# Performance work log

Measured on AMD Instinct MI355X. Metric: run time of the kernel, lower is better.

The kernel has to match this reference:

```python
import jax, jax.numpy as jnp
import numpy as np
import math

EMBED_DIM = 1024
NUM_HEADS = 16
HEAD_DIM = EMBED_DIM // NUM_HEADS


def setup_inputs() -> dict:
    key = jax.random.key(0)
    ks = jax.random.split(key, 5)
    x = jax.random.normal(ks[0], (4, 2048, EMBED_DIM), dtype=jnp.float32)
    # Linear params (torch nn.Linear: y = x @ W.T + b); init scale ~ 1/sqrt(fan_in)
    s = 1.0 / math.sqrt(EMBED_DIM)
    qkv_w = jax.random.uniform(ks[1], (3 * EMBED_DIM, EMBED_DIM), jnp.float32, -s, s)
    qkv_b = jax.random.uniform(ks[2], (3 * EMBED_DIM,), jnp.float32, -s, s)
    proj_w = jax.random.uniform(ks[3], (EMBED_DIM, EMBED_DIM), jnp.float32, -s, s)
    proj_b = jax.random.uniform(ks[4], (EMBED_DIM,), jnp.float32, -s, s)
    return {"x": x, "qkv_w": qkv_w, "qkv_b": qkv_b, "proj_w": proj_w, "proj_b": proj_b}


def reference(x, qkv_w, qkv_b, proj_w, proj_b):
    bsz, num_tokens, dim = x.shape
    qkv = x @ qkv_w.T + qkv_b  # [B, S, 3*D]
    qkv = qkv.reshape(bsz, num_tokens, 3, NUM_HEADS, HEAD_DIM)
    qkv = jnp.transpose(qkv, (2, 0, 3, 1, 4))  # [3, B, H, S, hd]
    q, k, v = qkv[0], qkv[1], qkv[2]
    scale = 1.0 / math.sqrt(HEAD_DIM)
    attn_scores = jnp.einsum('bhqd,bhkd->bhqk', q, k) * scale  # [B, H, S, S]
    attn = jax.nn.softmax(attn_scores, axis=-1)
    out = jnp.einsum('bhqk,bhkd->bhqd', attn, v)  # [B, H, S, hd]
    out = jnp.transpose(out, (0, 2, 1, 3)).reshape(bsz, num_tokens, dim)
    out = out @ proj_w.T + proj_b
    return out
```

## Files before the change

kernel.cpp:

```cpp
#include <hip/hip_runtime.h>
#include <stdint.h>

#define DEVICE static __device__ __forceinline__

typedef __bf16 bf16x8 __attribute__((ext_vector_type(8)));
typedef float f32x4 __attribute__((ext_vector_type(4)));

#define AS1 __attribute__((address_space(1)))
#define AS3 __attribute__((address_space(3)))

DEVICE void g2l16(const void* gptr, void* lptr) {
  __builtin_amdgcn_global_load_lds((AS1 uint32_t*)(uintptr_t)gptr,
                                   (AS3 uint32_t*)(uint32_t)(uintptr_t)lptr,
                                   16, 0, 0);
}

DEVICE float b2f(ushort h) {
  union { uint32_t u; float f; } v;
  v.u = ((uint32_t)h) << 16;
  return v.f;
}
DEVICE ushort f2b(float f) {
  union { float f; uint32_t u; } v;
  v.f = f;
  uint32_t u = v.u;
  return (ushort)((u + 0x7FFFu + ((u >> 16) & 1u)) >> 16);
}

#if defined(__has_builtin) && __has_builtin(__builtin_amdgcn_exp2f)
DEVICE float fast_exp2(float x) { return __builtin_amdgcn_exp2f(x); }
#else
extern "C" __device__ float __ocml_native_exp2_f32(float);
DEVICE float fast_exp2(float x) { return __ocml_native_exp2_f32(x); }
#endif

#define QSCALE 0.1803368801111244f

DEVICE int kperm(int x) {
  return (x & 0x23) | ((x & 0x18) >> 1) | ((x & 0x4) << 2);
}

__global__ void detect_dtype(const ushort* __restrict__ xu, int* __restrict__ flag) {
  __shared__ int bad;
  if (threadIdx.x == 0) bad = 0;
  __syncthreads();
  int mybad = 0;
#pragma unroll
  for (int j = 0; j < 8; ++j) {
    const int i = threadIdx.x * 8 + j;
    const ushort u = xu[2 * i];
    const int e = (u >> 7) & 0xFF;
    if (!(e == 0 || (e >= 96 && e <= 160))) mybad++;
  }
  atomicAdd(&bad, mybad);
  __syncthreads();
  if (threadIdx.x == 0) *flag = (bad > 512) ? 1 : 0;
}

__global__ void convert_all(const void* __restrict__ s0, const void* __restrict__ s1,
                            const void* __restrict__ s2, const void* __restrict__ s3,
                            const void* __restrict__ s4,
                            ushort* __restrict__ d0, ushort* __restrict__ d1,
                            ushort* __restrict__ d2, ushort* __restrict__ d3,
                            ushort* __restrict__ d4,
                            const int* __restrict__ flag) {
  const bool isf32 = (*flag != 0);
  for (int g = blockIdx.x * blockDim.x + threadIdx.x; g < 1573376;
       g += gridDim.x * blockDim.x) {
    const void* src; ushort* dst; int i;
    if (g < 1048576)      { src = s0; dst = d0; i = g; }
    else if (g < 1441792) { src = s1; dst = d1; i = g - 1048576; }
    else if (g < 1442176) { src = s2; dst = d2; i = g - 1441792; }
    else if (g < 1573248) { src = s3; dst = d3; i = g - 1442176; }
    else                  { src = s4; dst = d4; i = g - 1573248; }
    ushort pk[8];
    if (isf32) {
      const float4 a = ((const float4*)src)[2 * i];
      const float4 b = ((const float4*)src)[2 * i + 1];
      pk[0] = f2b(a.x); pk[1] = f2b(a.y); pk[2] = f2b(a.z); pk[3] = f2b(a.w);
      pk[4] = f2b(b.x); pk[5] = f2b(b.y); pk[6] = f2b(b.z); pk[7] = f2b(b.w);
      *(uint4*)&dst[8 * i] = *(const uint4*)pk;
    } else {
      *(uint4*)&dst[8 * i] = ((const uint4*)src)[i];
    }
  }
}

template <int MODE, int GN>
__global__ __launch_bounds__(512, 4)
void gemm256(const ushort* __restrict__ A, const ushort* __restrict__ W,
             const ushort* __restrict__ bias, ushort* __restrict__ O0,
             ushort* __restrict__ O1, ushort* __restrict__ O2,
             int M, int N, int K, const int* __restrict__ flag)
{
  __shared__ __align__(16) char smem[49152];

  const int tid = threadIdx.x;
  const int lane = tid & 63;
  const int wave = tid >> 6;
  const int quad = lane >> 4;
  const int lo = lane & 15;
  const int kch = (quad ^ ((lo >> 1) & 3)) << 3;

  const int lin = blockIdx.y * gridDim.x + blockIdx.x;
  const int per = GN * gridDim.y;
  const int grp = lin / per;
  const int w   = lin % per;
  const int bxn = grp * GN + (w % GN);
  const int bym = w / GN;
  const int m0 = bym * 128;
  const int n0 = bxn * 256;

  const int wm = (wave >> 2) * 64;
  const int wn = (wave & 3) * 64;

  const int rA = tid >> 2;
  const int gA = (((tid & 3) ^ ((tid >> 3) & 3)) << 3);
  const size_t offA  = (size_t)(m0 + rA) * K + gA;
  const size_t offB0 = (size_t)(n0 + rA) * K + gA;
  const size_t offB1 = (size_t)(n0 + 128 + rA) * K + gA;
  const int dA = wave << 10;
  const int NT = K >> 5;

  f32x4 acc[4][4] = {};

  g2l16(A + offA,  smem + dA);
  g2l16(W + offB0, smem + 8192 + dA);
  g2l16(W + offB1, smem + 16384 + dA);
  asm volatile("s_waitcnt vmcnt(0)" ::: "memory");
  __builtin_amdgcn_s_barrier();

  for (int kt = 0; kt < NT; ++kt) {
    const char* buf = smem + (kt & 1) * 24576;
    const ushort* Al = (const ushort*)buf;
    const ushort* Bl = (const ushort*)(buf + 8192);
    const bool pf = (kt + 1 < NT);
    char* nbuf = smem + ((kt + 1) & 1) * 24576;
    const size_t nk = (size_t)(kt + 1) * 32;

    if (pf) {
      g2l16(A + offA  + nk, nbuf + dA);
      g2l16(W + offB0 + nk, nbuf + 8192 + dA);
    }
    bf16x8 bfr[4], af[2];
#pragma unroll
    for (int nt = 0; nt < 4; ++nt)
      bfr[nt] = *(const bf16x8*)&Bl[(wn + nt * 16 + lo) * 32 + kch];
#pragma unroll
    for (int mt = 0; mt < 2; ++mt)
      af[mt] = *(const bf16x8*)&Al[(wm + mt * 16 + lo) * 32 + kch];
    __builtin_amdgcn_s_setprio(1);
#pragma unroll
    for (int mt = 0; mt < 2; ++mt)
#pragma unroll
      for (int nt = 0; nt < 4; ++nt)
        acc[mt][nt] = __builtin_amdgcn_mfma_f32_16x16x32_bf16(
            af[mt], bfr[nt], acc[mt][nt], 0, 0, 0);
    __builtin_amdgcn_s_setprio(0);
    __builtin_amdgcn_s_barrier();

    if (pf)
      g2l16(W + offB1 + nk, nbuf + 16384 + dA);
    bf16x8 af2[2];
#pragma unroll
    for (int mt = 0; mt < 2; ++mt)
      af2[mt] = *(const bf16x8*)&Al[(wm + (mt + 2) * 16 + lo) * 32 + kch];
    __builtin_amdgcn_s_setprio(1);
#pragma unroll
    for (int mt = 0; mt < 2; ++mt)
#pragma unroll
      for (int nt = 0; nt < 4; ++nt)
        acc[mt + 2][nt] = __builtin_amdgcn_mfma_f32_16x16x32_bf16(
            af2[mt], bfr[nt], acc[mt + 2][nt], 0, 0, 0);
    __builtin_amdgcn_s_setprio(0);

    if (kt < NT - 1) {
      asm volatile("s_waitcnt vmcnt(0)" ::: "memory");
      __builtin_amdgcn_s_barrier();
    }
  }

  if (MODE == 0) {
    const int which = n0 >> 10;
    if (which == 2) {
#pragma unroll
      for (int nt = 0; nt < 4; ++nt) {
        const int n = n0 + wn + nt * 16 + lo;
        const float bv = b2f(bias[n]);
        const int h = (n >> 6) & 15;
        const int d = n & 63;
#pragma unroll
        for (int mt = 0; mt < 4; ++mt) {
          const int m = m0 + wm + mt * 16 + quad * 4;
          const int b = m >> 11, s0 = m & 2047;
          ushort pk[4];
#pragma unroll
          for (int r = 0; r < 4; ++r) pk[r] = f2b(acc[mt][nt][r] + bv);
          *(uint2*)&O2[((size_t)(b * 16 + h) * 64 + d) * 2048 + s0] =
              *(const uint2*)pk;
        }
      }
    } else {
      const float qs = (which == 0) ? QSCALE : 1.0f;
      ushort* __restrict__ dst = (which == 0) ? O0 : O1;
      const int h = ((n0 + wn) >> 6) & 15;
      __syncthreads();
      ushort* scr = (ushort*)(smem + wave * 5632);
      float bv[4];
#pragma unroll
      for (int nt = 0; nt < 4; ++nt) bv[nt] = b2f(bias[n0 + wn + nt * 16 + lo]);
#pragma unroll
      for (int c2 = 0; c2 < 2; ++c2) {
#pragma unroll
        for (int mtl = 0; mtl < 2; ++mtl)
#pragma unroll
          for (int nt = 0; nt < 4; ++nt)
#pragma unroll
            for (int r = 0; r < 4; ++r)
              scr[(mtl * 16 + quad * 4 + r) * 88 + nt * 16 + lo] =
                  f2b((acc[c2 * 2 + mtl][nt][r] + bv[nt]) * qs);
        asm volatile("s_waitcnt lgkmcnt(0)" ::: "memory");
#pragma unroll
        for (int i = 0; i < 4; ++i) {
          const int id = lane + 64 * i;
          const int rowl = id >> 3, nch = id & 7;
          const uint4 val = *(const uint4*)&scr[rowl * 88 + nch * 8];
          const int m = m0 + wm + c2 * 32 + rowl;
          const int b = m >> 11;
          int s = m & 2047;
          if (which == 1) s = (s & ~63) | kperm(s & 63);
          *(uint4*)&dst[((size_t)(b * 16 + h) * 2048 + s) * 64 + nch * 8] = val;
        }
      }
    }
  } else {
    const bool f32out = (*flag != 0);
    float* Of = (float*)O0;
#pragma unroll
    for (int nt = 0; nt < 4; ++nt) {
      const int n = n0 + wn + nt * 16 + lo;
      const float bv = b2f(bias[n]);
#pragma unroll
      for (int mt = 0; mt < 4; ++mt)
#pragma unroll
        for (int r = 0; r < 4; ++r) {
          const int m = m0 + wm + mt * 16 + quad * 4 + r;
          const float val = acc[mt][nt][r] + bv;
          if (f32out) Of[(size_t)m * N + n] = val;
          else        O0[(size_t)m * N + n] = f2b(val);
        }
    }
  }
}

__global__ __launch_bounds__(256, 4)
void attn_fwd(const ushort* __restrict__ qp, const ushort* __restrict__ kp,
              const ushort* __restrict__ vp, ushort* __restrict__ o)
{
  __shared__ ushort Qs[128 * 64];
  __shared__ ushort Ks2[2][64 * 64];
  __shared__ ushort Vt2[2][64 * 64];

  const int tid = threadIdx.x;
  const int lane = tid & 63;
  const int wave = tid >> 6;
  const int quad = lane >> 4;
  const int lo = lane & 15;
  const int sw = (lo & 7) << 3;

  const int lin = blockIdx.y * gridDim.x + blockIdx.x;
  const int bh = (lin & 7) * 8 + ((lin >> 3) & 7);
  const int q0 = (lin >> 6) * 128;

  const ushort* Qg = qp + (size_t)bh * 2048 * 64;
  const ushort* Kg = kp + (size_t)bh * 2048 * 64;
  const ushort* Vg = vp + (size_t)bh * 64 * 2048;

#pragma unroll
  for (int i = 0; i < 4; ++i) {
    const int c = tid + 256 * i;
    const int row = c >> 3;
    const int kc = ((c ^ row) & 7) << 3;
    g2l16(Qg + (size_t)(q0 + row) * 64 + kc,
          (char*)Qs + ((wave << 6) + (i << 8)) * 16);
  }
#pragma unroll
  for (int i = 0; i < 2; ++i) {
    const int c = tid + 256 * i;
    const int row = c >> 3;
    const int kc = ((c ^ row) & 7) << 3;
    g2l16(Kg + (size_t)row * 64 + kc,
          (char*)Ks2[0] + ((wave << 6) + (i << 8)) * 16);
    g2l16(Vg + (size_t)row * 2048 + kc,
          (char*)Vt2[0] + ((wave << 6) + (i << 8)) * 16);
  }
  asm volatile("s_waitcnt vmcnt(0)" ::: "memory");
  __builtin_amdgcn_s_barrier();

  bf16x8 qf[2][2];
#pragma unroll
  for (int mt = 0; mt < 2; ++mt)
#pragma unroll
    for (int ks = 0; ks < 2; ++ks)
      qf[mt][ks] = *(const bf16x8*)&Qs[(wave * 32 + mt * 16 + lo) * 64 +
                                       ((ks * 32 + quad * 8) ^ sw)];

  bf16x8 ones;
#pragma unroll
  for (int j = 0; j < 8; ++j) ones[j] = (__bf16)1.0f;

  f32x4 oacc[2][4] = {};
  f32x4 sumacc[2] = {};

  for (int t = 0; t < 32; ++t) {
    const int cur = t & 1;
    const ushort* Kc = Ks2[cur];
    const ushort* Vc = Vt2[cur];

    if (t < 31) {
      const int j1 = (t + 1) * 64;
#pragma unroll
      for (int i = 0; i < 2; ++i) {
        const int c = tid + 256 * i;
        const int row = c >> 3;
        const int kc = ((c ^ row) & 7) << 3;
        g2l16(Kg + (size_t)(j1 + row) * 64 + kc,
              (char*)Ks2[cur ^ 1] + ((wave << 6) + (i << 8)) * 16);
        g2l16(Vg + (size_t)row * 2048 + j1 + kc,
              (char*)Vt2[cur ^ 1] + ((wave << 6) + (i << 8)) * 16);
      }
    }

    f32x4 sacc[2][4] = {};
#pragma unroll
    for (int ks = 0; ks < 2; ++ks) {
#pragma unroll
      for (int nt = 0; nt < 4; ++nt) {
        const bf16x8 kf =
            *(const bf16x8*)&Kc[(nt * 16 + lo) * 64 + ((ks * 32 + quad * 8) ^ sw)];
#pragma unroll
        for (int mt = 0; mt < 2; ++mt)
          sacc[mt][nt] = __builtin_amdgcn_mfma_f32_16x16x32_bf16(
              kf, qf[mt][ks], sacc[mt][nt], 0, 0, 0);
      }
    }

    bf16x8 pfr[2][2];
#pragma unroll
    for (int mt = 0; mt < 2; ++mt) {
      float p[4][4];
#pragma unroll
      for (int nt = 0; nt < 4; ++nt)
#pragma unroll
        for (int r = 0; r < 4; ++r)
          p[nt][r] = fast_exp2(sacc[mt][nt][r]);
#pragma unroll
      for (int b = 0; b < 2; ++b)
#pragma unroll
        for (int h = 0; h < 2; ++h)
#pragma unroll
          for (int r = 0; r < 4; ++r)
            pfr[mt][b][4 * h + r] = (__bf16)p[2 * b + h][r];
    }

#pragma unroll
    for (int b = 0; b < 2; ++b) {
#pragma unroll
      for (int mt = 0; mt < 2; ++mt)
        sumacc[mt] = __builtin_amdgcn_mfma_f32_16x16x32_bf16(
            pfr[mt][b], ones, sumacc[mt], 0, 0, 0);
#pragma unroll
      for (int dt = 0; dt < 4; ++dt) {
        const bf16x8 vf =
            *(const bf16x8*)&Vc[(dt * 16 + lo) * 64 + ((b * 32 + quad * 8) ^ sw)];
#pragma unroll
        for (int mt = 0; mt < 2; ++mt)
          oacc[mt][dt] = __builtin_amdgcn_mfma_f32_16x16x32_bf16(
              pfr[mt][b], vf, oacc[mt][dt], 0, 0, 0);
      }
    }

    asm volatile("s_waitcnt vmcnt(0)" ::: "memory");
    __builtin_amdgcn_s_barrier();
  }

  const int b_ = bh >> 4;
  const int h = bh & 15;
#pragma unroll
  for (int mt = 0; mt < 2; ++mt) {
#pragma unroll
    for (int r = 0; r < 4; ++r) {
      const float inv = 1.0f / sumacc[mt][r];
      const int srow = q0 + wave * 32 + mt * 16 + quad * 4 + r;
#pragma unroll
      for (int dt = 0; dt < 4; ++dt) {
        o[(((size_t)(b_ * 2048 + srow)) << 10) + h * 64 + dt * 16 + lo] =
            f2b(oacc[mt][dt][r] * inv);
      }
    }
  }
}

extern "C" void kernel_launch(void* const* d_in, const int* in_sizes, int n_in,
                              void* d_out, int out_size, void* d_ws, size_t ws_size,
                              hipStream_t stream) {
  const size_t N_X  = (size_t)4 * 2048 * 1024;
  const size_t N_WQ = (size_t)3072 * 1024;
  const size_t N_BQ = 3072;
  const size_t N_WP = (size_t)1024 * 1024;
  const size_t N_BP = 1024;
  const size_t HSD  = (size_t)64 * 2048 * 64;

  ushort* xb = (ushort*)d_ws;
  ushort* wq = xb + N_X;
  ushort* bq = wq + N_WQ;
  ushort* wp = bq + N_BQ;
  ushort* bp = wp + N_WP;
  ushort* qb = bp + N_BP;
  ushort* kb = qb + HSD;
  ushort* vb = kb + HSD;
  ushort* ab = vb + HSD;
  int* flag  = (int*)(ab + HSD);

  detect_dtype<<<1, 256, 0, stream>>>((const ushort*)d_in[0], flag);
  convert_all<<<2048, 256, 0, stream>>>(d_in[0], d_in[1], d_in[2], d_in[3], d_in[4],
                                        xb, wq, bq, wp, bp, flag);

  gemm256<0, 4><<<dim3(12, 64), dim3(512), 0, stream>>>(
      xb, wq, bq, qb, kb, vb, 8192, 3072, 1024, flag);
  attn_fwd<<<dim3(16, 64), dim3(256), 0, stream>>>(qb, kb, vb, ab);
  gemm256<1, 4><<<dim3(4, 64), dim3(512), 0, stream>>>(
      ab, wp, bp, (ushort*)d_out, nullptr, nullptr, 8192, 1024, 1024, flag);
}
```

Before: 279.6 us.

## Halve output-projection GEMM M-tile and reuse Q smem for K/V double buffer

The GEMM is templated on the M-tile count so the output projection uses 64-row tiles, doubling its grid from 256 to 512 blocks to fill more CUs. Only half the threads load the A tile in that mode. The attention kernel frees a separate K/V buffer by reusing the Q staging area as the second K/V buffer once Q fragments are in registers, which lowers LDS use per block so more blocks can be resident. This costs an extra barrier and less per-block reuse of the B tile in the projection GEMM.

After: 270.6 us. 3.2% less time.

```diff
diff --git a/kernel.cpp b/kernel.cpp
--- a/kernel.cpp
+++ b/kernel.cpp
@@ -86,14 +86,18 @@
   }
 }
 
-template <int MODE, int GN>
+template <int MODE, int GN, int MT>
 __global__ __launch_bounds__(512, 4)
 void gemm256(const ushort* __restrict__ A, const ushort* __restrict__ W,
              const ushort* __restrict__ bias, ushort* __restrict__ O0,
              ushort* __restrict__ O1, ushort* __restrict__ O2,
              int M, int N, int K, const int* __restrict__ flag)
 {
-  __shared__ __align__(16) char smem[49152];
+  constexpr int BM = MT * 32;
+  constexpr int ABYTES = BM * 64;
+  constexpr int BUFB = ABYTES + 16384;
+  constexpr int SMEMB = (MODE == 0) ? 49152 : 2 * BUFB;
+  __shared__ __align__(16) char smem[SMEMB];
 
   const int tid = threadIdx.x;
   const int lane = tid & 63;
@@ -108,10 +112,10 @@
   const int w   = lin % per;
   const int bxn = grp * GN + (w % GN);
   const int bym = w / GN;
-  const int m0 = bym * 128;
+  const int m0 = bym * BM;
   const int n0 = bxn * 256;
 
-  const int wm = (wave >> 2) * 64;
+  const int wm = (wave >> 2) * (MT * 16);
   const int wn = (wave & 3) * 64;
 
   const int rA = tid >> 2;
@@ -120,38 +124,43 @@
   const size_t offB0 = (size_t)(n0 + rA) * K + gA;
   const size_t offB1 = (size_t)(n0 + 128 + rA) * K + gA;
   const int dA = wave << 10;
+  const bool aload = (MT == 4) || (tid < 256);
   const int NT = K >> 5;
 
-  f32x4 acc[4][4] = {};
-
-  g2l16(A + offA,  smem + dA);
-  g2l16(W + offB0, smem + 8192 + dA);
-  g2l16(W + offB1, smem + 16384 + dA);
+  f32x4 acc[MT][4];
+#pragma unroll
+  for (int mt = 0; mt < MT; ++mt)
+#pragma unroll
+    for (int nt = 0; nt < 4; ++nt) acc[mt][nt] = (f32x4){0.f, 0.f, 0.f, 0.f};
+
+  if (aload) g2l16(A + offA, smem + dA);
+  g2l16(W + offB0, smem + ABYTES + dA);
+  g2l16(W + offB1, smem + ABYTES + 8192 + dA);
   asm volatile("s_waitcnt vmcnt(0)" ::: "memory");
   __builtin_amdgcn_s_barrier();
 
   for (int kt = 0; kt < NT; ++kt) {
-    const char* buf = smem + (kt & 1) * 24576;
+    const char* buf = smem + (kt & 1) * BUFB;
     const ushort* Al = (const ushort*)buf;
-    const ushort* Bl = (const ushort*)(buf + 8192);
+    const ushort* Bl = (const ushort*)(buf + ABYTES);
     const bool pf = (kt + 1 < NT);
-    char* nbuf = smem + ((kt + 1) & 1) * 24576;
+    char* nbuf = smem + ((kt + 1) & 1) * BUFB;
     const size_t nk = (size_t)(kt + 1) * 32;
 
     if (pf) {
-      g2l16(A + offA  + nk, nbuf + dA);
-      g2l16(W + offB0 + nk, nbuf + 8192 + dA);
-    }
-    bf16x8 bfr[4], af[2];
+      if (aload) g2l16(A + offA + nk, nbuf + dA);
+      g2l16(W + offB0 + nk, nbuf + ABYTES + dA);
+    }
+    bf16x8 bfr[4], af[MT / 2];
 #pragma unroll
     for (int nt = 0; nt < 4; ++nt)
       bfr[nt] = *(const bf16x8*)&Bl[(wn + nt * 16 + lo) * 32 + kch];
 #pragma unroll
-    for (int mt = 0; mt < 2; ++mt)
+    for (int mt = 0; mt < MT / 2; ++mt)
       af[mt] = *(const bf16x8*)&Al[(wm + mt * 16 + lo) * 32 + kch];
     __builtin_amdgcn_s_setprio(1);
 #pragma unroll
-    for (int mt = 0; mt < 2; ++mt)
+    for (int mt = 0; mt < MT / 2; ++mt)
 #pragma unroll
       for (int nt = 0; nt < 4; ++nt)
         acc[mt][nt] = __builtin_amdgcn_mfma_f32_16x16x32_bf16(
@@ -160,18 +169,18 @@
     __builtin_amdgcn_s_barrier();
 
     if (pf)
-      g2l16(W + offB1 + nk, nbuf + 16384 + dA);
-    bf16x8 af2[2];
-#pragma unroll
-    for (int mt = 0; mt < 2; ++mt)
-      af2[mt] = *(const bf16x8*)&Al[(wm + (mt + 2) * 16 + lo) * 32 + kch];
+      g2l16(W + offB1 + nk, nbuf + ABYTES + 8192 + dA);
+    bf16x8 af2[MT / 2];
+#pragma unroll
+    for (int mt = 0; mt < MT / 2; ++mt)
+      af2[mt] = *(const bf16x8*)&Al[(wm + (mt + MT / 2) * 16 + lo) * 32 + kch];
     __builtin_amdgcn_s_setprio(1);
 #pragma unroll
-    for (int mt = 0; mt < 2; ++mt)
+    for (int mt = 0; mt < MT / 2; ++mt)
 #pragma unroll
       for (int nt = 0; nt < 4; ++nt)
-        acc[mt + 2][nt] = __builtin_amdgcn_mfma_f32_16x16x32_bf16(
-            af2[mt], bfr[nt], acc[mt + 2][nt], 0, 0, 0);
+        acc[mt + MT / 2][nt] = __builtin_amdgcn_mfma_f32_16x16x32_bf16(
+            af2[mt], bfr[nt], acc[mt + MT / 2][nt], 0, 0, 0);
     __builtin_amdgcn_s_setprio(0);
 
     if (kt < NT - 1) {
@@ -190,7 +199,7 @@
         const int h = (n >> 6) & 15;
         const int d = n & 63;
 #pragma unroll
-        for (int mt = 0; mt < 4; ++mt) {
+        for (int mt = 0; mt < MT; ++mt) {
           const int m = m0 + wm + mt * 16 + quad * 4;
           const int b = m >> 11, s0 = m & 2047;
           ushort pk[4];
@@ -210,7 +219,7 @@
 #pragma unroll
       for (int nt = 0; nt < 4; ++nt) bv[nt] = b2f(bias[n0 + wn + nt * 16 + lo]);
 #pragma unroll
-      for (int c2 = 0; c2 < 2; ++c2) {
+      for (int c2 = 0; c2 < MT / 2; ++c2) {
 #pragma unroll
         for (int mtl = 0; mtl < 2; ++mtl)
 #pragma unroll
@@ -241,7 +250,7 @@
       const int n = n0 + wn + nt * 16 + lo;
       const float bv = b2f(bias[n]);
 #pragma unroll
-      for (int mt = 0; mt < 4; ++mt)
+      for (int mt = 0; mt < MT; ++mt)
 #pragma unroll
         for (int r = 0; r < 4; ++r) {
           const int m = m0 + wm + mt * 16 + quad * 4 + r;
@@ -257,9 +266,8 @@
 void attn_fwd(const ushort* __restrict__ qp, const ushort* __restrict__ kp,
               const ushort* __restrict__ vp, ushort* __restrict__ o)
 {
-  __shared__ ushort Qs[128 * 64];
-  __shared__ ushort Ks2[2][64 * 64];
-  __shared__ ushort Vt2[2][64 * 64];
+  __shared__ ushort SA[128 * 64];
+  __shared__ ushort SB[2][64 * 64];
 
   const int tid = threadIdx.x;
   const int lane = tid & 63;
@@ -282,7 +290,7 @@
     const int row = c >> 3;
     const int kc = ((c ^ row) & 7) << 3;
     g2l16(Qg + (size_t)(q0 + row) * 64 + kc,
-          (char*)Qs + ((wave << 6) + (i << 8)) * 16);
+          (char*)SA + ((wave << 6) + (i << 8)) * 16);
   }
 #pragma unroll
   for (int i = 0; i < 2; ++i) {
@@ -290,9 +298,9 @@
     const int row = c >> 3;
     const int kc = ((c ^ row) & 7) << 3;
     g2l16(Kg + (size_t)row * 64 + kc,
-          (char*)Ks2[0] + ((wave << 6) + (i << 8)) * 16);
+          (char*)SB[0] + ((wave << 6) + (i << 8)) * 16);
     g2l16(Vg + (size_t)row * 2048 + kc,
-          (char*)Vt2[0] + ((wave << 6) + (i << 8)) * 16);
+          (char*)SB[1] + ((wave << 6) + (i << 8)) * 16);
   }
   asm volatile("s_waitcnt vmcnt(0)" ::: "memory");
   __builtin_amdgcn_s_barrier();
@@ -302,8 +310,10 @@
   for (int mt = 0; mt < 2; ++mt)
 #pragma unroll
     for (int ks = 0; ks < 2; ++ks)
-      qf[mt][ks] = *(const bf16x8*)&Qs[(wave * 32 + mt * 16 + lo) * 64 +
+      qf[mt][ks] = *(const bf16x8*)&SA[(wave * 32 + mt * 16 + lo) * 64 +
                                        ((ks * 32 + quad * 8) ^ sw)];
+
+  __syncthreads();
 
   bf16x8 ones;
 #pragma unroll
@@ -314,8 +324,10 @@
 
   for (int t = 0; t < 32; ++t) {
     const int cur = t & 1;
-    const ushort* Kc = Ks2[cur];
-    const ushort* Vc = Vt2[cur];
+    const ushort* Kc = cur ? SA : SB[0];
+    const ushort* Vc = cur ? (SA + 64 * 64) : SB[1];
+    char* Kn = (char*)(cur ? SB[0] : SA);
+    char* Vn = (char*)(cur ? SB[1] : (SA + 64 * 64));
 
     if (t < 31) {
       const int j1 = (t + 1) * 64;
@@ -325,9 +337,9 @@
         const int row = c >> 3;
         const int kc = ((c ^ row) & 7) << 3;
         g2l16(Kg + (size_t)(j1 + row) * 64 + kc,
-              (char*)Ks2[cur ^ 1] + ((wave << 6) + (i << 8)) * 16);
+              Kn + ((wave << 6) + (i << 8)) * 16);
         g2l16(Vg + (size_t)row * 2048 + j1 + kc,
-              (char*)Vt2[cur ^ 1] + ((wave << 6) + (i << 8)) * 16);
+              Vn + ((wave << 6) + (i << 8)) * 16);
       }
     }
 
@@ -426,9 +438,9 @@
   convert_all<<<2048, 256, 0, stream>>>(d_in[0], d_in[1], d_in[2], d_in[3], d_in[4],
                                         xb, wq, bq, wp, bp, flag);
 
-  gemm256<0, 4><<<dim3(12, 64), dim3(512), 0, stream>>>(
+  gemm256<0, 4, 4><<<dim3(12, 64), dim3(512), 0, stream>>>(
       xb, wq, bq, qb, kb, vb, 8192, 3072, 1024, flag);
   attn_fwd<<<dim3(16, 64), dim3(256), 0, stream>>>(qb, kb, vb, ab);
-  gemm256<1, 4><<<dim3(4, 64), dim3(512), 0, stream>>>(
+  gemm256<1, 4, 2><<<dim3(4, 128), dim3(512), 0, stream>>>(
       ab, wp, bp, (ushort*)d_out, nullptr, nullptr, 8192, 1024, 1024, flag);
 }
```
